# Kernel tuning notes

Hardware: AMD Instinct MI355X
Metric: run time of the kernel (lower is better)

Reference implementation:

```python
import jax, jax.numpy as jnp
import numpy as np

B, N_Z, N_E, D = 16, 2048, 2048, 512

def setup_inputs() -> dict:
    key = jax.random.key(0)
    kz, ke, km = jax.random.split(key, 3)
    z = jax.random.normal(kz, (B, N_Z, D), dtype=jnp.float32)
    e = jax.random.normal(ke, (B, N_E, D), dtype=jnp.float32)
    M = jax.random.normal(km, (D, D), dtype=jnp.float32)  # init: normal(0, 1)
    return {"z": z, "e": e, "M": M}

def reference(z, e, M):
    # a = z @ M @ e^T : [B, Nz, Ne]
    zM = jnp.einsum('bnd,de->bne', z, M)
    a = jnp.einsum('bnd,bmd->bnm', zM, e)
    a = jax.nn.sigmoid(a)
    # softmax over dim=1 (the Nz axis), as in the torch code
    A = jax.nn.softmax(a, axis=1)
    # out = A @ e : [B, Nz, D]
    return jnp.einsum('bnm,bmd->bnd', A, e)
```

## Files before the change

### kernel.cpp

```cpp
#include <hip/hip_runtime.h>
#include <hip/hip_bf16.h>
#include <stdint.h>

#define BB 16
#define NZ 2048
#define NE 2048
#define DD 512

typedef unsigned short u16;
typedef __attribute__((ext_vector_type(8))) _Float16 f16x8;
typedef __attribute__((ext_vector_type(4))) float f32x4;

__device__ __forceinline__ u16 f2h(float f) {
  _Float16 h = (_Float16)f;
  return __builtin_bit_cast(u16, h);
}

__device__ __forceinline__ float h2f(u16 h) {
  return (float)__builtin_bit_cast(_Float16, h);
}

__device__ __forceinline__ void gload_lds16(const void* g, void* l) {
  auto gp = (const __attribute__((address_space(1))) uint32_t*)g;
  auto lp = (__attribute__((address_space(3))) uint32_t*)l;
  __builtin_amdgcn_global_load_lds(gp, lp, 16, 0, 0);
}

#define FENCE() asm volatile("" ::: "memory")
#define BARRIER() do { FENCE(); __builtin_amdgcn_s_barrier(); FENCE(); } while (0)
#define WAIT_VM(n) asm volatile("s_waitcnt vmcnt(" #n ")" ::: "memory")

__global__ void k_cvt(const float* __restrict__ in, u16* __restrict__ out, int n4) {
  int i = blockIdx.x * blockDim.x + threadIdx.x;
  int stride = gridDim.x * blockDim.x;
  for (; i < n4; i += stride) {
    float4 v = ((const float4*)in)[i];
    ushort4 o;
    o.x = f2h(v.x); o.y = f2h(v.y); o.z = f2h(v.z); o.w = f2h(v.w);
    ((ushort4*)out)[i] = o;
  }
}

__global__ void k_mt(const float* __restrict__ M, u16* __restrict__ Mt) {
  __shared__ float t[32][33];
  int bx = blockIdx.x * 32;
  int by = blockIdx.y * 32;
  for (int r = 0; r < 32; r += 8)
    t[threadIdx.y + r][threadIdx.x] = M[(size_t)(by + threadIdx.y + r) * DD + bx + threadIdx.x];
  __syncthreads();
  for (int r = 0; r < 32; r += 8)
    Mt[(size_t)(bx + threadIdx.y + r) * DD + by + threadIdx.x] = f2h(t[threadIdx.x][threadIdx.y + r]);
}

__global__ void k_et(const u16* __restrict__ eH, const float* __restrict__ cs,
                     u16* __restrict__ eT) {
  __shared__ float t[32][33];
  int b = blockIdx.z;
  int m0 = blockIdx.y * 32, d0 = blockIdx.x * 32;
  const u16* eb = eH + (size_t)b * NE * DD;
  const float* csb = cs + (size_t)b * NE;
  for (int r = 0; r < 32; r += 8) {
    int m = m0 + threadIdx.y + r;
    t[threadIdx.y + r][threadIdx.x] =
        h2f(eb[(size_t)m * DD + d0 + threadIdx.x]) * (2048.0f / csb[m]);
  }
  __syncthreads();
  u16* eTb = eT + (size_t)b * DD * NE;
  for (int r = 0; r < 32; r += 8) {
    int d = d0 + threadIdx.y + r;
    eTb[(size_t)d * NE + m0 + threadIdx.x] = f2h(t[threadIdx.x][threadIdx.y + r]);
  }
}

template<int EPI, int KDIM>
__global__ __launch_bounds__(512, 2) void k_gemm(
    const u16* __restrict__ A, const u16* __restrict__ Bt, void* __restrict__ Cp,
    int Ndim, long long sAb, long long sBb, long long sCb,
    float* __restrict__ colsum, int csld)
{
  extern __shared__ char lds[];
  constexpr int NT = KDIM / 64;

  const int gx = gridDim.x, gy = gridDim.y;
  const int nwg = gx * gy * gridDim.z;
  const int hid = blockIdx.x + gx * (blockIdx.y + gy * blockIdx.z);
  const int logical = (hid & 7) * (nwg >> 3) + (hid >> 3);
  const int bx = logical % gx;
  const int rem0 = logical / gx;
  const int by = rem0 % gy;
  const int bz = rem0 / gy;

  const int tid = threadIdx.x;
  const int lane = tid & 63;
  const int wid = tid >> 6;
  const int wr = wid >> 2;
  const int wc = wid & 3;

  const int row0 = by * 256;
  const int col0 = bx * 256;

  const u16* Ab = A + (long long)bz * sAb;
  const u16* Bb = Bt + (long long)bz * sBb;

  const u16* srcA[4]; const u16* srcB[4];
#pragma unroll
  for (int c = 0; c < 4; ++c) {
    int idx = c * 512 + tid;
    int ks = idx >> 10;
    int r = (idx & 1023) >> 2;
    int cL = idx & 3;
    int q = ks * 4 + (cL ^ ((r >> 1) & 3));
    srcA[c] = Ab + (long long)(row0 + r) * KDIM + q * 8;
    srcB[c] = Bb + (long long)(col0 + r) * KDIM + q * 8;
  }

  auto stage = [&](int buf, int k0) {
    char* dA = lds + buf * 32768;
    char* dB = lds + 65536 + buf * 32768;
#pragma unroll
    for (int c = 0; c < 2; ++c) gload_lds16(srcA[c] + k0, dA + (c * 512 + wid * 64) * 16);
#pragma unroll
    for (int c = 0; c < 2; ++c) gload_lds16(srcB[c] + k0, dB + (c * 512 + wid * 64) * 16);
#pragma unroll
    for (int c = 2; c < 4; ++c) gload_lds16(srcA[c] + k0, dA + (c * 512 + wid * 64) * 16);
#pragma unroll
    for (int c = 2; c < 4; ++c) gload_lds16(srcB[c] + k0, dB + (c * 512 + wid * 64) * 16);
  };

  auto ldA = [&](int buf, int ks, int m) -> f16x8 {
    int r = wr * 128 + m * 16 + (lane & 15);
    int c4 = (lane >> 4) ^ ((r >> 1) & 3);
    return *(const f16x8*)(lds + buf * 32768 + ks * 16384 + r * 64 + c4 * 16);
  };
  auto ldB = [&](int buf, int ks, int n) -> f16x8 {
    int r = wc * 64 + n * 16 + (lane & 15);
    int c4 = (lane >> 4) ^ ((r >> 1) & 3);
    return *(const f16x8*)(lds + 65536 + buf * 32768 + ks * 16384 + r * 64 + c4 * 16);
  };

  f32x4 acc[8][4] = {};

  stage(0, 0);
  WAIT_VM(4);
  BARRIER();

  for (int t = 0; t < NT; ++t) {
    const int buf = t & 1;
    const bool pf = (t + 1 < NT);
    if (pf) stage(buf ^ 1, (t + 1) * 64);

    {
      f16x8 af[8], bf[4];
#pragma unroll
      for (int m = 0; m < 8; ++m) af[m] = ldA(buf, 0, m);
#pragma unroll
      for (int n = 0; n < 4; ++n) bf[n] = ldB(buf, 0, n);
#pragma unroll
      for (int m = 0; m < 8; ++m)
#pragma unroll
        for (int n = 0; n < 4; ++n)
          acc[m][n] = __builtin_amdgcn_mfma_f32_16x16x32_f16(af[m], bf[n], acc[m][n], 0, 0, 0);
    }
    if (pf) { WAIT_VM(8); } else { WAIT_VM(0); }
    BARRIER();

    {
      f16x8 af[8], bf[4];
#pragma unroll
      for (int m = 0; m < 8; ++m) af[m] = ldA(buf, 1, m);
#pragma unroll
      for (int n = 0; n < 4; ++n) bf[n] = ldB(buf, 1, n);
#pragma unroll
      for (int m = 0; m < 8; ++m)
#pragma unroll
        for (int n = 0; n < 4; ++n)
          acc[m][n] = __builtin_amdgcn_mfma_f32_16x16x32_f16(af[m], bf[n], acc[m][n], 0, 0, 0);
    }
    if (pf) {
      WAIT_VM(4);
      BARRIER();
    }
  }

  __syncthreads();

  const int rr = (lane >> 4) * 4;
  const int cc = lane & 15;
  const int grow = row0 + wr * 128;
  const int gcol = col0 + wc * 64;

  if constexpr (EPI == 0 || EPI == 1) {
    char* wb = lds + wid * 16384;
    float csum[4] = {0.f, 0.f, 0.f, 0.f};
#pragma unroll
    for (int m = 0; m < 8; ++m)
#pragma unroll
      for (int n = 0; n < 4; ++n)
#pragma unroll
        for (int j = 0; j < 4; ++j) {
          float x = acc[m][n][j];
          float v;
          if constexpr (EPI == 1) {
            float s = 1.f / (1.f + __expf(-x));
            v = __expf(s);
            csum[n] += v;
          } else {
            v = x;
          }
          int rl = m * 16 + rr + j;
          int col = n * 16 + cc;
          int chunk = (col >> 3) ^ (rl & 7);
          *(u16*)(wb + rl * 128 + chunk * 16 + ((col * 2) & 15)) = f2h(v);
        }
    if constexpr (EPI == 1) {
#pragma unroll
      for (int n = 0; n < 4; ++n) {
        float v = csum[n];
        v += __shfl_xor(v, 16, 64);
        v += __shfl_xor(v, 32, 64);
        if ((lane >> 4) == 0)
          atomicAdd(&colsum[(long long)bz * csld + gcol + n * 16 + cc], v);
      }
    }
    __syncthreads();
    u16* C = (u16*)Cp + (long long)bz * sCb;
#pragma unroll
    for (int s = 0; s < 16; ++s) {
      int rl = (lane >> 3) + s * 8;
      int chunk = (lane & 7) ^ (rl & 7);
      f16x8 v = *(const f16x8*)(wb + rl * 128 + chunk * 16);
      *(f16x8*)(&C[(long long)(grow + rl) * Ndim + gcol + (lane & 7) * 8]) = v;
    }
  } else {
    float* C = (float*)Cp + (long long)bz * sCb;
    char* wb = lds + wid * 16384;
#pragma unroll
    for (int h = 0; h < 2; ++h) {
      if (h) __syncthreads();
#pragma unroll
      for (int mm = 0; mm < 4; ++mm) {
        int m = h * 4 + mm;
#pragma unroll
        for (int n = 0; n < 4; ++n)
#pragma unroll
          for (int j = 0; j < 4; ++j) {
            int rl = mm * 16 + rr + j;
            int col = n * 16 + cc;
            int chunk = (col >> 2) ^ (rl & 15);
            *(float*)(wb + rl * 256 + chunk * 16 + ((col * 4) & 15)) =
                acc[m][n][j] * (1.0f / 2048.0f);
          }
      }
      __syncthreads();
#pragma unroll
      for (int s = 0; s < 16; ++s) {
        int rl = (lane >> 4) + s * 4;
        int chunk = (lane & 15) ^ (rl & 15);
        f32x4 v = *(const f32x4*)(wb + rl * 256 + chunk * 16);
        *(f32x4*)(&C[(long long)(grow + h * 64 + rl) * Ndim + gcol + (lane & 15) * 4]) = v;
      }
    }
  }
}

extern "C" void kernel_launch(void* const* d_in, const int* in_sizes, int n_in,
                              void* d_out, int out_size, void* d_ws, size_t ws_size,
                              hipStream_t stream) {
  const float* z = (const float*)d_in[0];
  const float* e = (const float*)d_in[1];
  const float* M = (const float*)d_in[2];
  float* out = (float*)d_out;
  char* ws = (char*)d_ws;

  u16* S    = (u16*)(ws + 0LL);
  u16* zM   = (u16*)(ws + 134217728LL);
  u16* zH   = (u16*)(ws + 167772160LL);
  u16* eH   = (u16*)(ws + 201326592LL);
  u16* Mt   = (u16*)(ws + 234881024LL);
  float* cs = (float*)(ws + 235405312LL);

  (void)hipFuncSetAttribute(reinterpret_cast<const void*>(&k_gemm<0, 512>),
                            hipFuncAttributeMaxDynamicSharedMemorySize, 131072);
  (void)hipFuncSetAttribute(reinterpret_cast<const void*>(&k_gemm<1, 512>),
                            hipFuncAttributeMaxDynamicSharedMemorySize, 131072);
  (void)hipFuncSetAttribute(reinterpret_cast<const void*>(&k_gemm<2, 2048>),
                            hipFuncAttributeMaxDynamicSharedMemorySize, 131072);

  hipMemsetAsync(cs, 0, (size_t)BB * NE * sizeof(float), stream);

  k_cvt<<<4096, 256, 0, stream>>>(z, zH, BB * NZ * DD / 4);
  k_cvt<<<4096, 256, 0, stream>>>(e, eH, BB * NE * DD / 4);
  k_mt<<<dim3(16, 16), dim3(32, 8), 0, stream>>>(M, Mt);

  k_gemm<0, 512><<<dim3(DD / 256, (BB * NZ) / 256, 1), 512, 131072, stream>>>(
      zH, Mt, zM, DD, 0LL, 0LL, 0LL, nullptr, 0);

  k_gemm<1, 512><<<dim3(NE / 256, NZ / 256, BB), 512, 131072, stream>>>(
      zM, eH, S, NE,
      (long long)NZ * DD, (long long)NE * DD, (long long)NZ * NE, cs, NE);

  u16* eT = zH;
  k_et<<<dim3(DD / 32, NE / 32, BB), dim3(32, 8), 0, stream>>>(eH, cs, eT);

  k_gemm<2, 2048><<<dim3(DD / 256, NZ / 256, BB), 512, 131072, stream>>>(
      S, eT, out, DD,
      (long long)NZ * NE, (long long)DD * NE, (long long)NZ * DD, nullptr, 0);
}
```

Measured before the change: 274.5 us.

## Switch GEMM mainloop to 4-stage ring of K=32 tiles with prefetch depth two

Replaces the double-buffered K=64 staging, which waited and barriered twice per iteration, with a four-slot LDS ring of K=32 tiles that prefetches two tiles ahead and needs one barrier per step. The B fragments are loaded in two halves to reduce register pressure, and MFMA blocks are wrapped in s_setprio to favour the math wave during issue. The aim is deeper overlap of global-to-LDS loads with MFMA work. In exchange there are twice as many loop iterations and barriers per K, and reuse of the ring slots depends on the barrier ordering being correct.

```diff
diff --git a/kernel.cpp b/kernel.cpp
--- a/kernel.cpp
+++ b/kernel.cpp
@@ -79,7 +79,7 @@
     float* __restrict__ colsum, int csld)
 {
   extern __shared__ char lds[];
-  constexpr int NT = KDIM / 64;
+  constexpr int NT = KDIM / 32;
 
   const int gx = gridDim.x, gy = gridDim.y;
   const int nwg = gx * gy * gridDim.z;
@@ -102,84 +102,74 @@
   const u16* Ab = A + (long long)bz * sAb;
   const u16* Bb = Bt + (long long)bz * sBb;
 
-  const u16* srcA[4]; const u16* srcB[4];
-#pragma unroll
-  for (int c = 0; c < 4; ++c) {
+  const u16* srcA[2]; const u16* srcB[2];
+#pragma unroll
+  for (int c = 0; c < 2; ++c) {
     int idx = c * 512 + tid;
-    int ks = idx >> 10;
-    int r = (idx & 1023) >> 2;
+    int r = idx >> 2;
     int cL = idx & 3;
-    int q = ks * 4 + (cL ^ ((r >> 1) & 3));
+    int q = cL ^ ((r >> 1) & 3);
     srcA[c] = Ab + (long long)(row0 + r) * KDIM + q * 8;
     srcB[c] = Bb + (long long)(col0 + r) * KDIM + q * 8;
   }
 
-  auto stage = [&](int buf, int k0) {
-    char* dA = lds + buf * 32768;
-    char* dB = lds + 65536 + buf * 32768;
-#pragma unroll
-    for (int c = 0; c < 2; ++c) gload_lds16(srcA[c] + k0, dA + (c * 512 + wid * 64) * 16);
-#pragma unroll
-    for (int c = 0; c < 2; ++c) gload_lds16(srcB[c] + k0, dB + (c * 512 + wid * 64) * 16);
-#pragma unroll
-    for (int c = 2; c < 4; ++c) gload_lds16(srcA[c] + k0, dA + (c * 512 + wid * 64) * 16);
-#pragma unroll
-    for (int c = 2; c < 4; ++c) gload_lds16(srcB[c] + k0, dB + (c * 512 + wid * 64) * 16);
+  auto stage = [&](int t) {
+    const int k0 = t * 32;
+    char* d = lds + (t & 3) * 32768;
+#pragma unroll
+    for (int c = 0; c < 2; ++c)
+      gload_lds16(srcA[c] + k0, d + (c * 512 + wid * 64) * 16);
+#pragma unroll
+    for (int c = 0; c < 2; ++c)
+      gload_lds16(srcB[c] + k0, d + 16384 + (c * 512 + wid * 64) * 16);
   };
 
-  auto ldA = [&](int buf, int ks, int m) -> f16x8 {
-    int r = wr * 128 + m * 16 + (lane & 15);
-    int c4 = (lane >> 4) ^ ((r >> 1) & 3);
-    return *(const f16x8*)(lds + buf * 32768 + ks * 16384 + r * 64 + c4 * 16);
+  const int p15 = lane & 15;
+  const int hi = lane >> 4;
+
+  auto ldA = [&](int t, int m) -> f16x8 {
+    int r = wr * 128 + m * 16 + p15;
+    int c4 = hi ^ ((r >> 1) & 3);
+    return *(const f16x8*)(lds + (t & 3) * 32768 + r * 64 + c4 * 16);
   };
-  auto ldB = [&](int buf, int ks, int n) -> f16x8 {
-    int r = wc * 64 + n * 16 + (lane & 15);
-    int c4 = (lane >> 4) ^ ((r >> 1) & 3);
-    return *(const f16x8*)(lds + 65536 + buf * 32768 + ks * 16384 + r * 64 + c4 * 16);
+  auto ldB = [&](int t, int n) -> f16x8 {
+    int r = wc * 64 + n * 16 + p15;
+    int c4 = hi ^ ((r >> 1) & 3);
+    return *(const f16x8*)(lds + (t & 3) * 32768 + 16384 + r * 64 + c4 * 16);
   };
 
   f32x4 acc[8][4] = {};
 
-  stage(0, 0);
-  WAIT_VM(4);
-  BARRIER();
+  stage(0);
+  stage(1);
 
   for (int t = 0; t < NT; ++t) {
-    const int buf = t & 1;
-    const bool pf = (t + 1 < NT);
-    if (pf) stage(buf ^ 1, (t + 1) * 64);
-
-    {
-      f16x8 af[8], bf[4];
-#pragma unroll
-      for (int m = 0; m < 8; ++m) af[m] = ldA(buf, 0, m);
-#pragma unroll
-      for (int n = 0; n < 4; ++n) bf[n] = ldB(buf, 0, n);
-#pragma unroll
-      for (int m = 0; m < 8; ++m)
-#pragma unroll
-        for (int n = 0; n < 4; ++n)
-          acc[m][n] = __builtin_amdgcn_mfma_f32_16x16x32_f16(af[m], bf[n], acc[m][n], 0, 0, 0);
-    }
-    if (pf) { WAIT_VM(8); } else { WAIT_VM(0); }
+    if (t + 2 < NT) { stage(t + 2); WAIT_VM(8); }
+    else if (t + 1 < NT) { WAIT_VM(4); }
+    else { WAIT_VM(0); }
     BARRIER();
 
-    {
-      f16x8 af[8], bf[4];
-#pragma unroll
-      for (int m = 0; m < 8; ++m) af[m] = ldA(buf, 1, m);
-#pragma unroll
-      for (int n = 0; n < 4; ++n) bf[n] = ldB(buf, 1, n);
-#pragma unroll
-      for (int m = 0; m < 8; ++m)
-#pragma unroll
-        for (int n = 0; n < 4; ++n)
-          acc[m][n] = __builtin_amdgcn_mfma_f32_16x16x32_f16(af[m], bf[n], acc[m][n], 0, 0, 0);
-    }
-    if (pf) {
-      WAIT_VM(4);
-      BARRIER();
-    }
+    f16x8 af[8], bf[2];
+#pragma unroll
+    for (int m = 0; m < 8; ++m) af[m] = ldA(t, m);
+
+    bf[0] = ldB(t, 0); bf[1] = ldB(t, 1);
+    __builtin_amdgcn_s_setprio(1);
+#pragma unroll
+    for (int m = 0; m < 8; ++m) {
+      acc[m][0] = __builtin_amdgcn_mfma_f32_16x16x32_f16(af[m], bf[0], acc[m][0], 0, 0, 0);
+      acc[m][1] = __builtin_amdgcn_mfma_f32_16x16x32_f16(af[m], bf[1], acc[m][1], 0, 0, 0);
+    }
+    __builtin_amdgcn_s_setprio(0);
+
+    bf[0] = ldB(t, 2); bf[1] = ldB(t, 3);
+    __builtin_amdgcn_s_setprio(1);
+#pragma unroll
+    for (int m = 0; m < 8; ++m) {
+      acc[m][2] = __builtin_amdgcn_mfma_f32_16x16x32_f16(af[m], bf[0], acc[m][2], 0, 0, 0);
+      acc[m][3] = __builtin_amdgcn_mfma_f32_16x16x32_f16(af[m], bf[1], acc[m][3], 0, 0, 0);
+    }
+    __builtin_amdgcn_s_setprio(0);
   }
 
   __syncthreads();
```

Result: no change. 272.9 us (-0.6%).

## Interleave LDS fragment loads, async global prefetch and MFMA in four phases

Applied to the files above, without the earlier changes.

Restructures the GEMM main loop into four sub-phases per K tile. Each phase loads half the A fragments from LDS, issues a slice of the next tile's global-to-LDS prefetch, then runs a 4x4 MFMA block at raised wave priority via s_setprio. The aim is to keep the matrix units busy while LDS reads and global loads proceed, and to cut register pressure by holding 4 rather than 8 A fragments. In exchange it adds many more barriers per iteration and relies on fine-grained vmcnt accounting that must stay correct for the split staging.

```diff
diff --git a/kernel.cpp b/kernel.cpp
--- a/kernel.cpp
+++ b/kernel.cpp
@@ -28,6 +28,7 @@
 
 #define FENCE() asm volatile("" ::: "memory")
 #define BARRIER() do { FENCE(); __builtin_amdgcn_s_barrier(); FENCE(); } while (0)
+#define WAIT_LGKM0() asm volatile("s_waitcnt lgkmcnt(0)" ::: "memory")
 #define WAIT_VM(n) asm volatile("s_waitcnt vmcnt(" #n ")" ::: "memory")
 
 __global__ void k_cvt(const float* __restrict__ in, u16* __restrict__ out, int n4) {
@@ -114,72 +115,102 @@
     srcB[c] = Bb + (long long)(col0 + r) * KDIM + q * 8;
   }
 
-  auto stage = [&](int buf, int k0) {
-    char* dA = lds + buf * 32768;
-    char* dB = lds + 65536 + buf * 32768;
-#pragma unroll
-    for (int c = 0; c < 2; ++c) gload_lds16(srcA[c] + k0, dA + (c * 512 + wid * 64) * 16);
-#pragma unroll
-    for (int c = 0; c < 2; ++c) gload_lds16(srcB[c] + k0, dB + (c * 512 + wid * 64) * 16);
-#pragma unroll
-    for (int c = 2; c < 4; ++c) gload_lds16(srcA[c] + k0, dA + (c * 512 + wid * 64) * 16);
-#pragma unroll
-    for (int c = 2; c < 4; ++c) gload_lds16(srcB[c] + k0, dB + (c * 512 + wid * 64) * 16);
+  auto stageA = [&](int buf, int k0, int c0) {
+#pragma unroll
+    for (int c = c0; c < c0 + 2; ++c)
+      gload_lds16(srcA[c] + k0, lds + buf * 32768 + (c * 512 + wid * 64) * 16);
   };
+  auto stageB = [&](int buf, int k0, int c0) {
+#pragma unroll
+    for (int c = c0; c < c0 + 2; ++c)
+      gload_lds16(srcB[c] + k0, lds + 65536 + buf * 32768 + (c * 512 + wid * 64) * 16);
+  };
+
+  const int p15 = lane & 15;
+  const int hi = lane >> 4;
 
   auto ldA = [&](int buf, int ks, int m) -> f16x8 {
-    int r = wr * 128 + m * 16 + (lane & 15);
-    int c4 = (lane >> 4) ^ ((r >> 1) & 3);
-    return *(const f16x8*)(lds + buf * 32768 + ks * 16384 + r * 64 + c4 * 16);
+    int r = wr * 128 + m * 16 + p15;
+    int cw = hi ^ ((r >> 1) & 3);
+    return *(const f16x8*)(lds + buf * 32768 + ks * 16384 + r * 64 + cw * 16);
   };
   auto ldB = [&](int buf, int ks, int n) -> f16x8 {
-    int r = wc * 64 + n * 16 + (lane & 15);
-    int c4 = (lane >> 4) ^ ((r >> 1) & 3);
-    return *(const f16x8*)(lds + 65536 + buf * 32768 + ks * 16384 + r * 64 + c4 * 16);
+    int r = wc * 64 + n * 16 + p15;
+    int cw = hi ^ ((r >> 1) & 3);
+    return *(const f16x8*)(lds + 65536 + buf * 32768 + ks * 16384 + r * 64 + cw * 16);
   };
 
   f32x4 acc[8][4] = {};
-
-  stage(0, 0);
+  f16x8 af[4], bf[4];
+
+  stageA(0, 0, 0); stageB(0, 0, 0);
+  stageA(0, 0, 2); stageB(0, 0, 2);
   WAIT_VM(4);
   BARRIER();
 
   for (int t = 0; t < NT; ++t) {
     const int buf = t & 1;
     const bool pf = (t + 1 < NT);
-    if (pf) stage(buf ^ 1, (t + 1) * 64);
-
-    {
-      f16x8 af[8], bf[4];
-#pragma unroll
-      for (int m = 0; m < 8; ++m) af[m] = ldA(buf, 0, m);
-#pragma unroll
-      for (int n = 0; n < 4; ++n) bf[n] = ldB(buf, 0, n);
-#pragma unroll
-      for (int m = 0; m < 8; ++m)
-#pragma unroll
-        for (int n = 0; n < 4; ++n)
-          acc[m][n] = __builtin_amdgcn_mfma_f32_16x16x32_f16(af[m], bf[n], acc[m][n], 0, 0, 0);
-    }
-    if (pf) { WAIT_VM(8); } else { WAIT_VM(0); }
-    BARRIER();
-
-    {
-      f16x8 af[8], bf[4];
-#pragma unroll
-      for (int m = 0; m < 8; ++m) af[m] = ldA(buf, 1, m);
-#pragma unroll
-      for (int n = 0; n < 4; ++n) bf[n] = ldB(buf, 1, n);
-#pragma unroll
-      for (int m = 0; m < 8; ++m)
-#pragma unroll
-        for (int n = 0; n < 4; ++n)
-          acc[m][n] = __builtin_amdgcn_mfma_f32_16x16x32_f16(af[m], bf[n], acc[m][n], 0, 0, 0);
-    }
-    if (pf) {
-      WAIT_VM(4);
-      BARRIER();
-    }
+    const int nk = (t + 1) * 64;
+
+#pragma unroll
+    for (int m = 0; m < 4; ++m) af[m] = ldA(buf, 0, m);
+#pragma unroll
+    for (int n = 0; n < 4; ++n) bf[n] = ldB(buf, 0, n);
+    if (pf) stageA(buf ^ 1, nk, 0);
+    BARRIER();
+    WAIT_LGKM0();
+    __builtin_amdgcn_s_setprio(1);
+#pragma unroll
+    for (int m = 0; m < 4; ++m)
+#pragma unroll
+      for (int n = 0; n < 4; ++n)
+        acc[m][n] = __builtin_amdgcn_mfma_f32_16x16x32_f16(af[m], bf[n], acc[m][n], 0, 0, 0);
+    __builtin_amdgcn_s_setprio(0);
+    BARRIER();
+#pragma unroll
+    for (int m = 0; m < 4; ++m) af[m] = ldA(buf, 0, 4 + m);
+    if (pf) stageB(buf ^ 1, nk, 0);
+    BARRIER();
+    WAIT_LGKM0();
+    __builtin_amdgcn_s_setprio(1);
+#pragma unroll
+    for (int m = 0; m < 4; ++m)
+#pragma unroll
+      for (int n = 0; n < 4; ++n)
+        acc[4 + m][n] = __builtin_amdgcn_mfma_f32_16x16x32_f16(af[m], bf[n], acc[4 + m][n], 0, 0, 0);
+    __builtin_amdgcn_s_setprio(0);
+    if (pf) { WAIT_VM(4); } else { WAIT_VM(0); }
+    BARRIER();
+#pragma unroll
+    for (int m = 0; m < 4; ++m) af[m] = ldA(buf, 1, m);
+#pragma unroll
+    for (int n = 0; n < 4; ++n) bf[n] = ldB(buf, 1, n);
+    if (pf) stageA(buf ^ 1, nk, 2);
+    BARRIER();
+    WAIT_LGKM0();
+    __builtin_amdgcn_s_setprio(1);
+#pragma unroll
+    for (int m = 0; m < 4; ++m)
+#pragma unroll
+      for (int n = 0; n < 4; ++n)
+        acc[m][n] = __builtin_amdgcn_mfma_f32_16x16x32_f16(af[m], bf[n], acc[m][n], 0, 0, 0);
+    __builtin_amdgcn_s_setprio(0);
+    BARRIER();
+#pragma unroll
+    for (int m = 0; m < 4; ++m) af[m] = ldA(buf, 1, 4 + m);
+    if (pf) stageB(buf ^ 1, nk, 2);
+    BARRIER();
+    WAIT_LGKM0();
+    __builtin_amdgcn_s_setprio(1);
+#pragma unroll
+    for (int m = 0; m < 4; ++m)
+#pragma unroll
+      for (int n = 0; n < 4; ++n)
+        acc[4 + m][n] = __builtin_amdgcn_mfma_f32_16x16x32_f16(af[m], bf[n], acc[4 + m][n], 0, 0, 0);
+    __builtin_amdgcn_s_setprio(0);
+    if (pf) { WAIT_VM(4); }
+    BARRIER();
   }
 
   __syncthreads();
```

After: 278.0 us. Within noise of the previous version (+1.3%).
